# Kernel optimization log

Hardware: AMD Instinct MI355X
Metric: run time of the kernel (lower is better)

## Reference

```python
import jax, jax.numpy as jnp
import numpy as np

N_NODES = 100000
N_EDGES = 1600000
DIM = 128


def setup_inputs() -> dict:
    key = jax.random.key(0)
    k1, k2, k3, k4, k5 = jax.random.split(key, 5)
    x = jax.random.normal(k1, (N_NODES, DIM), dtype=jnp.float32)
    edge_index = jax.random.randint(k2, (2, N_EDGES), 0, N_NODES, dtype=jnp.int64)
    s = 1.0 / np.sqrt(DIM)
    W_lin = jax.random.uniform(k3, (DIM, DIM), jnp.float32, -s, s)   # nn.Linear (bias=False)
    W_gcn = jax.random.uniform(k4, (DIM, DIM), jnp.float32, -s, s)   # GCNConv internal lin (bias=False)
    b_gcn = jax.random.uniform(k5, (DIM,), jnp.float32, -s, s)       # GCNConv bias
    return {"x": x, "edge_index": edge_index, "W_lin": W_lin, "W_gcn": W_gcn, "b_gcn": b_gcn}


def reference(x, edge_index, W_lin, W_gcn, b_gcn):
    N = x.shape[0]
    # self.linear (bias=False) then GCNConv's internal linear (bias=False)
    h = (x @ W_lin.T) @ W_gcn.T                                      # [N, D]
    # add self loops (PyG GCNConv default add_self_loops=True)
    loop = jnp.arange(N, dtype=edge_index.dtype)
    row = jnp.concatenate([edge_index[0], loop])                     # source
    col = jnp.concatenate([edge_index[1], loop])                     # target
    # symmetric normalization: deg over targets incl. self loops
    deg = jax.ops.segment_sum(jnp.ones_like(col, dtype=h.dtype), col, num_segments=N)
    dinv = jnp.where(deg > 0, jax.lax.rsqrt(deg), 0.0)               # deg^{-1/2}, inf->0
    norm = dinv[row] * dinv[col]                                     # [E+N]
    # gather -> scale -> scatter-add (aggr='add', flow source_to_target)
    msg = h[row] * norm[:, None]                                     # [E+N, D]
    out = jax.ops.segment_sum(msg, col, num_segments=N) + b_gcn      # [N, D]
    # NOTE: self.relu is `Sequential as ReLU` -> empty Sequential -> identity
    return out
```

## Files before the change

kernel.cpp:

```cpp
#include <hip/hip_runtime.h>
#include <hip/hip_bf16.h>

#define DIM 128
#define NBUCK 2048
#define BCAP 1344

typedef short bf16x8 __attribute__((ext_vector_type(8)));
typedef float f32x4 __attribute__((ext_vector_type(4)));

__device__ __forceinline__ unsigned short f2bf(float f) {
    __hip_bfloat16 h = __float2bfloat16(f);
    return *reinterpret_cast<unsigned short*>(&h);
}
__device__ __forceinline__ float u2f(unsigned int u) {
    union { unsigned int i; float f; } v; v.i = u; return v.f;
}
__device__ __forceinline__ unsigned int f2u(float f) {
    union { float f; unsigned int i; } v; v.f = f; return v.i;
}

__global__ __launch_bounds__(128) void wp_kernel(const float* __restrict__ Wg,
                                                 const float* __restrict__ Wl,
                                                 unsigned short* __restrict__ Wpb,
                                                 int* __restrict__ bcur,
                                                 int* __restrict__ degi, int N) {
    const int c = blockIdx.x;
    const int k = threadIdx.x;
    const int gid = c * 128 + k;
    if (gid < NBUCK) bcur[gid] = 0;
    for (int i = gid; i < N; i += 128 * 128) degi[i] = 0;
    float s = 0.f;
    for (int j = 0; j < DIM; ++j)
        s = fmaf(Wg[c * DIM + j], Wl[j * DIM + k], s);
    Wpb[c * DIM + k] = f2bf(s);
}

__global__ __launch_bounds__(256) void part_gemm_kernel(
        const int* __restrict__ src, const int* __restrict__ dst,
        int* __restrict__ bcur, unsigned int* __restrict__ ebuf,
        int* __restrict__ degi, int E, int nchunk,
        const float* __restrict__ x, const unsigned short* __restrict__ Wpb,
        unsigned int* __restrict__ hbu, int N) {
    __shared__ __align__(16) char smem[49152];
    const int t = threadIdx.x;

    if (blockIdx.x < 256) {
        int* hist = (int*)smem;
        int* base = hist + NBUCK;
        for (int i = t; i < NBUCK; i += 256) hist[i] = 0;
        __syncthreads();

        const int e0 = blockIdx.x * nchunk;
        const int e1 = min(e0 + nchunk, E);
        for (int e = e0 + t; e < e1; e += 256) {
            const int d = dst[e];
            atomicAdd(&hist[d >> 6], 1);
            atomicAdd(&degi[d], 1);
        }
        __syncthreads();

        for (int i = t; i < NBUCK; i += 256) {
            const int cc = hist[i];
            base[i] = (cc > 0) ? atomicAdd(&bcur[i], cc) : 0;
        }
        __syncthreads();

        for (int e = e0 + t; e < e1; e += 256) {
            const int d = dst[e];
            const int b = d >> 6;
            const int pos = atomicAdd(&base[b], 1);
            if (pos < BCAP) {
                const unsigned int p = (unsigned int)src[e] | ((unsigned int)(d & 63) << 17);
                ebuf[(size_t)b * BCAP + pos] = p;
            }
        }
        return;
    }

    unsigned short* xs  = (unsigned short*)smem;
    unsigned short* wps = xs + 64 * 128;
    const int brow = (blockIdx.x - 256) * 64;

#pragma unroll
    for (int j = 0; j < 8; ++j) {
        const int col = (t >> 4) + j * 16;
        const int kb = t & 15;
        const uint4 v = *(const uint4*)(Wpb + col * 128 + kb * 8);
        *(uint4*)&wps[col * 128 + ((kb ^ (col & 15)) * 8)] = v;
    }
#pragma unroll
    for (int i = 0; i < 4; ++i) {
        const int row = (t >> 4) + i * 16;
        const int kb = t & 15;
        const int g = brow + row;
        float4 a0 = make_float4(0.f, 0.f, 0.f, 0.f), a1 = a0;
        if (g < N) {
            a0 = *(const float4*)(x + (size_t)g * 128 + kb * 8);
            a1 = *(const float4*)(x + (size_t)g * 128 + kb * 8 + 4);
        }
        ushort4 lo, hi;
        lo.x = f2bf(a0.x); lo.y = f2bf(a0.y); lo.z = f2bf(a0.z); lo.w = f2bf(a0.w);
        hi.x = f2bf(a1.x); hi.y = f2bf(a1.y); hi.z = f2bf(a1.z); hi.w = f2bf(a1.w);
        unsigned short* p = &xs[row * 128 + ((kb ^ (row & 15)) * 8)];
        *(ushort4*)p = lo;
        *(ushort4*)(p + 4) = hi;
    }
    __syncthreads();

    const int lane = t & 63, wv = t >> 6;
    const int m16 = lane & 15, quad = lane >> 4;

    f32x4 acc[8];
#pragma unroll
    for (int ct = 0; ct < 8; ++ct) acc[ct] = (f32x4){0.f, 0.f, 0.f, 0.f};

    const int arow = wv * 16 + m16;
#pragma unroll
    for (int s = 0; s < 4; ++s) {
        const int pk = ((s * 4 + quad) ^ m16) * 8;
        const bf16x8 a = *(const bf16x8*)&xs[arow * 128 + pk];
#pragma unroll
        for (int ct = 0; ct < 8; ++ct) {
            const bf16x8 b = *(const bf16x8*)&wps[(ct * 16 + m16) * 128 + pk];
            acc[ct] = __builtin_amdgcn_mfma_f32_16x16x32_bf16(a, b, acc[ct], 0, 0, 0);
        }
    }

    const int r0 = brow + wv * 16 + quad * 4;
#pragma unroll
    for (int ct = 0; ct < 4; ++ct) {
        const int col = ct * 16 + m16;
#pragma unroll
        for (int r = 0; r < 4; ++r) {
            if (r0 + r < N) {
                const unsigned int pk = (unsigned int)f2bf(acc[ct][r]) |
                                        ((unsigned int)f2bf(acc[ct + 4][r]) << 16);
                hbu[(size_t)(r0 + r) * 64 + col] = pk;
            }
        }
    }
}

__global__ __launch_bounds__(256) void sortgather_kernel(
        const unsigned int* __restrict__ hbu, const unsigned int* __restrict__ ebuf,
        const int* __restrict__ bcur, const int* __restrict__ degi,
        const float* __restrict__ b, float* __restrict__ out, int N) {
    __shared__ unsigned int pairs[BCAP * 2];
    __shared__ int cnt[64];
    __shared__ int scn[64];
    __shared__ int st[64];
    __shared__ int deg[64];
    const int t   = threadIdx.x;
    const int bkt = blockIdx.x;
    const int c   = min(bcur[bkt], BCAP);
    const unsigned int* eb = ebuf + (size_t)bkt * BCAP;

    if (t < 64) cnt[t] = 0;
    __syncthreads();

    for (int i = t; i < c; i += 256)
        atomicAdd(&cnt[eb[i] >> 17], 1);
    __syncthreads();

    if (t < 64) scn[t] = cnt[t];
    __syncthreads();
    for (int off = 1; off < 64; off <<= 1) {
        int v = (t < 64 && t >= off) ? scn[t - off] : 0;
        __syncthreads();
        if (t < 64) scn[t] += v;
        __syncthreads();
    }
    if (t < 64) {
        const int excl = scn[t] - cnt[t];
        st[t]  = excl;
        deg[t] = cnt[t];
        cnt[t] = excl;
    }
    __syncthreads();

    for (int i = t; i < c; i += 256) {
        const unsigned int p = eb[i];
        const int s = (int)(p & 0x1FFFF);
        const int pos = atomicAdd(&cnt[p >> 17], 1);
        const float g = rsqrtf((float)(degi[s] + 1));
        uint2 pr; pr.x = (unsigned int)s; pr.y = f2u(g);
        *(uint2*)&pairs[2 * pos] = pr;
    }
    __syncthreads();

    const int lane = t & 63;
    const int wv   = t >> 6;
    const float bx = b[lane];
    const float by = b[lane + 64];
    const int n0 = bkt << 6;

    for (int i = 0; i < 16; ++i) {
        const int dl = wv * 16 + i;
        const int node = n0 + dl;
        if (node >= N) continue;
        const int dgi = deg[dl];
        const float dv = rsqrtf((float)(dgi + 1));
        const unsigned int self = hbu[(size_t)node * 64 + lane];
        float ax = dv * u2f(self << 16);
        float ay = dv * u2f(self & 0xFFFF0000u);

        const int jb = st[dl];
        const int je = jb + dgi;
        int j = jb;
        for (; j + 4 <= je; j += 4) {
            const uint2 p0 = *(const uint2*)&pairs[2 * (j + 0)];
            const uint2 p1 = *(const uint2*)&pairs[2 * (j + 1)];
            const uint2 p2 = *(const uint2*)&pairs[2 * (j + 2)];
            const uint2 p3 = *(const uint2*)&pairs[2 * (j + 3)];
            const unsigned int v0 = hbu[(size_t)p0.x * 64 + lane];
            const unsigned int v1 = hbu[(size_t)p1.x * 64 + lane];
            const unsigned int v2 = hbu[(size_t)p2.x * 64 + lane];
            const unsigned int v3 = hbu[(size_t)p3.x * 64 + lane];
            const float g0 = u2f(p0.y), g1 = u2f(p1.y), g2 = u2f(p2.y), g3 = u2f(p3.y);
            ax = fmaf(u2f(v0 << 16), g0, ax);
            ax = fmaf(u2f(v1 << 16), g1, ax);
            ax = fmaf(u2f(v2 << 16), g2, ax);
            ax = fmaf(u2f(v3 << 16), g3, ax);
            ay = fmaf(u2f(v0 & 0xFFFF0000u), g0, ay);
            ay = fmaf(u2f(v1 & 0xFFFF0000u), g1, ay);
            ay = fmaf(u2f(v2 & 0xFFFF0000u), g2, ay);
            ay = fmaf(u2f(v3 & 0xFFFF0000u), g3, ay);
        }
        for (; j < je; ++j) {
            const uint2 pr = *(const uint2*)&pairs[2 * j];
            const unsigned int v = hbu[(size_t)pr.x * 64 + lane];
            const float g = u2f(pr.y);
            ax = fmaf(u2f(v << 16), g, ax);
            ay = fmaf(u2f(v & 0xFFFF0000u), g, ay);
        }
        out[(size_t)node * 128 + lane]      = dv * ax + bx;
        out[(size_t)node * 128 + 64 + lane] = dv * ay + by;
    }
}

extern "C" void kernel_launch(void* const* d_in, const int* in_sizes, int n_in,
                              void* d_out, int out_size, void* d_ws, size_t ws_size,
                              hipStream_t stream) {
    const float* x  = (const float*)d_in[0];
    const int*   ei = (const int*)d_in[1];
    const float* Wl = (const float*)d_in[2];
    const float* Wg = (const float*)d_in[3];
    const float* bg = (const float*)d_in[4];

    const int N = in_sizes[0] / DIM;
    const int E = in_sizes[1] / 2;
    const int* srcIdx = ei;
    const int* dstIdx = ei + E;

    char* wsb = (char*)d_ws;
    unsigned short* Wpb  = (unsigned short*)(wsb + 0);
    int*            bcur = (int*)(wsb + 65536);
    int*            degi = (int*)(wsb + 131072);
    unsigned int*   ebuf = (unsigned int*)(wsb + 2097152);
    unsigned int*   hbu  = (unsigned int*)(wsb + 16777216);
    const size_t needed = 16777216ull + (size_t)N * DIM * 2;
    if (ws_size < needed) return;

    const int nbkt = (N + 63) >> 6;
    const int ngemm = (N + 63) / 64;
    const int nchunk = (E + 255) / 256;

    wp_kernel        <<<DIM, DIM, 0, stream>>>(Wg, Wl, Wpb, bcur, degi, N);
    part_gemm_kernel <<<256 + ngemm, 256, 0, stream>>>(srcIdx, dstIdx, bcur, ebuf, degi,
                                                       E, nchunk, x, Wpb, hbu, N);
    sortgather_kernel<<<nbkt, 256, 0, stream>>>(hbu, ebuf, bcur, degi, bg,
                                                (float*)d_out, N);
}
```

Measured before the change: 270.4 us.

## Compute degrees from bucketed edges in separate pass, precompute dinv, unroll gather by 8

The 1.6M global atomic degree increments in the partition pass are removed. A new per-bucket kernel counts in-degrees from the already-bucketed edge buffer in shared memory and writes both the degree and a precomputed deg^-1/2 array. The sort-gather kernel then reads these values instead of recounting and recomputing rsqrt per edge, and its gather loop is unrolled from 4 to 8 to keep more loads in flight. The cost is an extra kernel launch and one more read pass over ebuf.

```diff
diff --git a/kernel.cpp b/kernel.cpp
--- a/kernel.cpp
+++ b/kernel.cpp
@@ -22,13 +22,11 @@
 __global__ __launch_bounds__(128) void wp_kernel(const float* __restrict__ Wg,
                                                  const float* __restrict__ Wl,
                                                  unsigned short* __restrict__ Wpb,
-                                                 int* __restrict__ bcur,
-                                                 int* __restrict__ degi, int N) {
+                                                 int* __restrict__ bcur) {
     const int c = blockIdx.x;
     const int k = threadIdx.x;
     const int gid = c * 128 + k;
     if (gid < NBUCK) bcur[gid] = 0;
-    for (int i = gid; i < N; i += 128 * 128) degi[i] = 0;
     float s = 0.f;
     for (int j = 0; j < DIM; ++j)
         s = fmaf(Wg[c * DIM + j], Wl[j * DIM + k], s);
@@ -38,7 +36,7 @@
 __global__ __launch_bounds__(256) void part_gemm_kernel(
         const int* __restrict__ src, const int* __restrict__ dst,
         int* __restrict__ bcur, unsigned int* __restrict__ ebuf,
-        int* __restrict__ degi, int E, int nchunk,
+        int E, int nchunk,
         const float* __restrict__ x, const unsigned short* __restrict__ Wpb,
         unsigned int* __restrict__ hbu, int N) {
     __shared__ __align__(16) char smem[49152];
@@ -52,11 +50,8 @@
 
         const int e0 = blockIdx.x * nchunk;
         const int e1 = min(e0 + nchunk, E);
-        for (int e = e0 + t; e < e1; e += 256) {
-            const int d = dst[e];
-            atomicAdd(&hist[d >> 6], 1);
-            atomicAdd(&degi[d], 1);
-        }
+        for (int e = e0 + t; e < e1; e += 256)
+            atomicAdd(&hist[dst[e] >> 6], 1);
         __syncthreads();
 
         for (int i = t; i < NBUCK; i += 256) {
@@ -141,9 +136,33 @@
     }
 }
 
+__global__ __launch_bounds__(256) void bcount_kernel(const unsigned int* __restrict__ ebuf,
+                                                     const int* __restrict__ bcur,
+                                                     int* __restrict__ degi,
+                                                     float* __restrict__ dinv, int N) {
+    __shared__ int cnt[64];
+    const int t = threadIdx.x;
+    const int bkt = blockIdx.x;
+    if (t < 64) cnt[t] = 0;
+    __syncthreads();
+    const int c = min(bcur[bkt], BCAP);
+    const unsigned int* eb = ebuf + (size_t)bkt * BCAP;
+    for (int i = t; i < c; i += 256)
+        atomicAdd(&cnt[eb[i] >> 17], 1);
+    __syncthreads();
+    if (t < 64) {
+        const int node = (bkt << 6) + t;
+        if (node < N) {
+            degi[node] = cnt[t];
+            dinv[node] = rsqrtf((float)(cnt[t] + 1));
+        }
+    }
+}
+
 __global__ __launch_bounds__(256) void sortgather_kernel(
         const unsigned int* __restrict__ hbu, const unsigned int* __restrict__ ebuf,
         const int* __restrict__ bcur, const int* __restrict__ degi,
+        const float* __restrict__ dinv,
         const float* __restrict__ b, float* __restrict__ out, int N) {
     __shared__ unsigned int pairs[BCAP * 2];
     __shared__ int cnt[64];
@@ -154,15 +173,14 @@
     const int bkt = blockIdx.x;
     const int c   = min(bcur[bkt], BCAP);
     const unsigned int* eb = ebuf + (size_t)bkt * BCAP;
-
-    if (t < 64) cnt[t] = 0;
-    __syncthreads();
-
-    for (int i = t; i < c; i += 256)
-        atomicAdd(&cnt[eb[i] >> 17], 1);
-    __syncthreads();
-
-    if (t < 64) scn[t] = cnt[t];
+    const int n0 = bkt << 6;
+
+    if (t < 64) {
+        const int node = n0 + t;
+        const int d = (node < N) ? degi[node] : 0;
+        deg[t] = d;
+        scn[t] = d;
+    }
     __syncthreads();
     for (int off = 1; off < 64; off <<= 1) {
         int v = (t < 64 && t >= off) ? scn[t - off] : 0;
@@ -171,9 +189,8 @@
         __syncthreads();
     }
     if (t < 64) {
-        const int excl = scn[t] - cnt[t];
+        const int excl = scn[t] - deg[t];
         st[t]  = excl;
-        deg[t] = cnt[t];
         cnt[t] = excl;
     }
     __syncthreads();
@@ -182,8 +199,7 @@
         const unsigned int p = eb[i];
         const int s = (int)(p & 0x1FFFF);
         const int pos = atomicAdd(&cnt[p >> 17], 1);
-        const float g = rsqrtf((float)(degi[s] + 1));
-        uint2 pr; pr.x = (unsigned int)s; pr.y = f2u(g);
+        uint2 pr; pr.x = (unsigned int)s; pr.y = f2u(dinv[s]);
         *(uint2*)&pairs[2 * pos] = pr;
     }
     __syncthreads();
@@ -192,7 +208,6 @@
     const int wv   = t >> 6;
     const float bx = b[lane];
     const float by = b[lane + 64];
-    const int n0 = bkt << 6;
 
     for (int i = 0; i < 16; ++i) {
         const int dl = wv * 16 + i;
@@ -207,31 +222,55 @@
         const int jb = st[dl];
         const int je = jb + dgi;
         int j = jb;
-        for (; j + 4 <= je; j += 4) {
+        for (; j + 8 <= je; j += 8) {
             const uint2 p0 = *(const uint2*)&pairs[2 * (j + 0)];
             const uint2 p1 = *(const uint2*)&pairs[2 * (j + 1)];
             const uint2 p2 = *(const uint2*)&pairs[2 * (j + 2)];
             const uint2 p3 = *(const uint2*)&pairs[2 * (j + 3)];
+            const uint2 p4 = *(const uint2*)&pairs[2 * (j + 4)];
+            const uint2 p5 = *(const uint2*)&pairs[2 * (j + 5)];
+            const uint2 p6 = *(const uint2*)&pairs[2 * (j + 6)];
+            const uint2 p7 = *(const uint2*)&pairs[2 * (j + 7)];
             const unsigned int v0 = hbu[(size_t)p0.x * 64 + lane];
             const unsigned int v1 = hbu[(size_t)p1.x * 64 + lane];
             const unsigned int v2 = hbu[(size_t)p2.x * 64 + lane];
             const unsigned int v3 = hbu[(size_t)p3.x * 64 + lane];
-            const float g0 = u2f(p0.y), g1 = u2f(p1.y), g2 = u2f(p2.y), g3 = u2f(p3.y);
-            ax = fmaf(u2f(v0 << 16), g0, ax);
-            ax = fmaf(u2f(v1 << 16), g1, ax);
-            ax = fmaf(u2f(v2 << 16), g2, ax);
-            ax = fmaf(u2f(v3 << 16), g3, ax);
-            ay = fmaf(u2f(v0 & 0xFFFF0000u), g0, ay);
-            ay = fmaf(u2f(v1 & 0xFFFF0000u), g1, ay);
-            ay = fmaf(u2f(v2 & 0xFFFF0000u), g2, ay);
-            ay = fmaf(u2f(v3 & 0xFFFF0000u), g3, ay);
+            const unsigned int v4 = hbu[(size_t)p4.x * 64 + lane];
+            const unsigned int v5 = hbu[(size_t)p5.x * 64 + lane];
+            const unsigned int v6 = hbu[(size_t)p6.x * 64 + lane];
+            const unsigned int v7 = hbu[(size_t)p7.x * 64 + lane];
+            ax = fmaf(u2f(v0 << 16), u2f(p0.y), ax);
+            ax = fmaf(u2f(v1 << 16), u2f(p1.y), ax);
+            ax = fmaf(u2f(v2 << 16), u2f(p2.y), ax);
+            ax = fmaf(u2f(v3 << 16), u2f(p3.y), ax);
+            ax = fmaf(u2f(v4 << 16), u2f(p4.y), ax);
+            ax = fmaf(u2f(v5 << 16), u2f(p5.y), ax);
+            ax = fmaf(u2f(v6 << 16), u2f(p6.y), ax);
+            ax = fmaf(u2f(v7 << 16), u2f(p7.y), ax);
+            ay = fmaf(u2f(v0 & 0xFFFF0000u), u2f(p0.y), ay);
+            ay = fmaf(u2f(v1 & 0xFFFF0000u), u2f(p1.y), ay);
+            ay = fmaf(u2f(v2 & 0xFFFF0000u), u2f(p2.y), ay);
+            ay = fmaf(u2f(v3 & 0xFFFF0000u), u2f(p3.y), ay);
+            ay = fmaf(u2f(v4 & 0xFFFF0000u), u2f(p4.y), ay);
+            ay = fmaf(u2f(v5 & 0xFFFF0000u), u2f(p5.y), ay);
+            ay = fmaf(u2f(v6 & 0xFFFF0000u), u2f(p6.y), ay);
+            ay = fmaf(u2f(v7 & 0xFFFF0000u), u2f(p7.y), ay);
+        }
+        for (; j + 2 <= je; j += 2) {
+            const uint2 p0 = *(const uint2*)&pairs[2 * (j + 0)];
+            const uint2 p1 = *(const uint2*)&pairs[2 * (j + 1)];
+            const unsigned int v0 = hbu[(size_t)p0.x * 64 + lane];
+            const unsigned int v1 = hbu[(size_t)p1.x * 64 + lane];
+            ax = fmaf(u2f(v0 << 16), u2f(p0.y), ax);
+            ax = fmaf(u2f(v1 << 16), u2f(p1.y), ax);
+            ay = fmaf(u2f(v0 & 0xFFFF0000u), u2f(p0.y), ay);
+            ay = fmaf(u2f(v1 & 0xFFFF0000u), u2f(p1.y), ay);
         }
         for (; j < je; ++j) {
             const uint2 pr = *(const uint2*)&pairs[2 * j];
             const unsigned int v = hbu[(size_t)pr.x * 64 + lane];
-            const float g = u2f(pr.y);
-            ax = fmaf(u2f(v << 16), g, ax);
-            ay = fmaf(u2f(v & 0xFFFF0000u), g, ay);
+            ax = fmaf(u2f(v << 16), u2f(pr.y), ax);
+            ay = fmaf(u2f(v & 0xFFFF0000u), u2f(pr.y), ay);
         }
         out[(size_t)node * 128 + lane]      = dv * ax + bx;
         out[(size_t)node * 128 + 64 + lane] = dv * ay + by;
@@ -256,6 +295,7 @@
     unsigned short* Wpb  = (unsigned short*)(wsb + 0);
     int*            bcur = (int*)(wsb + 65536);
     int*            degi = (int*)(wsb + 131072);
+    float*          dinv = (float*)(wsb + 589824);
     unsigned int*   ebuf = (unsigned int*)(wsb + 2097152);
     unsigned int*   hbu  = (unsigned int*)(wsb + 16777216);
     const size_t needed = 16777216ull + (size_t)N * DIM * 2;
@@ -265,9 +305,10 @@
     const int ngemm = (N + 63) / 64;
     const int nchunk = (E + 255) / 256;
 
-    wp_kernel        <<<DIM, DIM, 0, stream>>>(Wg, Wl, Wpb, bcur, degi, N);
-    part_gemm_kernel <<<256 + ngemm, 256, 0, stream>>>(srcIdx, dstIdx, bcur, ebuf, degi,
+    wp_kernel        <<<DIM, DIM, 0, stream>>>(Wg, Wl, Wpb, bcur);
+    part_gemm_kernel <<<256 + ngemm, 256, 0, stream>>>(srcIdx, dstIdx, bcur, ebuf,
                                                        E, nchunk, x, Wpb, hbu, N);
-    sortgather_kernel<<<nbkt, 256, 0, stream>>>(hbu, ebuf, bcur, degi, bg,
+    bcount_kernel    <<<nbkt, 256, 0, stream>>>(ebuf, bcur, degi, dinv, N);
+    sortgather_kernel<<<nbkt, 256, 0, stream>>>(hbu, ebuf, bcur, degi, dinv, bg,
                                                 (float*)d_out, N);
 }
```

New measurement: 221.2 us. 1.22x faster.
